# Kernel optimization log

Hardware: AMD Instinct MI355X
Metric: run time of the kernel (lower is better)

The kernel has to match this reference:

```python
import jax, jax.numpy as jnp
import numpy as np

NUM_GRAPHS = 64


def setup_inputs() -> dict:
    key = jax.random.key(0)
    ks = jax.random.split(key, 8)
    N, E, H, D_IN, NEXP = 100000, 1600000, 128, 4, 8
    atomic_numbers = jax.random.uniform(ks[0], (N,), dtype=jnp.float32) * 80.0
    pos = jax.random.normal(ks[1], (N, 3), dtype=jnp.float32)
    W0 = jax.random.normal(ks[2], (D_IN, H), dtype=jnp.float32) / np.sqrt(D_IN)
    b0 = jnp.zeros((H,), dtype=jnp.float32)
    W1 = jax.random.normal(ks[3], (H, H), dtype=jnp.float32) / np.sqrt(H)
    b1 = jnp.zeros((H,), dtype=jnp.float32)
    W2 = jax.random.normal(ks[4], (H, H), dtype=jnp.float32) / np.sqrt(H)
    b2 = jnp.zeros((H,), dtype=jnp.float32)
    lin_W = jax.random.normal(ks[5], (H, NEXP), dtype=jnp.float32) / np.sqrt(H)
    lin_b = jnp.zeros((NEXP,), dtype=jnp.float32)
    edge_index = jax.random.randint(ks[6], (2, E), 0, N, dtype=jnp.int64)
    batch = jnp.sort(jax.random.randint(ks[7], (N,), 0, NUM_GRAPHS, dtype=jnp.int64))
    return {
        "atomic_numbers": atomic_numbers, "pos": pos,
        "W0": W0, "b0": b0, "W1": W1, "b1": b1, "W2": W2, "b2": b2,
        "lin_W": lin_W, "lin_b": lin_b,
        "edge_index": edge_index, "batch": batch,
    }


def _gcn_layer(x, W, b, src, dst, norm, num_nodes):
    # GCNConv: transform, then symmetric-normalized scatter-aggregate (self-loops included in src/dst)
    h = x @ W                                   # [N, H]
    msg = h[src] * norm[:, None]                # [E+N, H] edge-gather
    out = jax.ops.segment_sum(msg, dst, num_segments=num_nodes)  # scatter-add at targets
    return out + b


def reference(atomic_numbers, pos, W0, b0, W1, b1, W2, b2, lin_W, lin_b, edge_index, batch):
    N = atomic_numbers.shape[0]
    x = jnp.concatenate([atomic_numbers[:, None], pos], axis=-1)  # [N, 4]

    # add self-loops (PyG GCNConv default)
    loop = jnp.arange(N, dtype=edge_index.dtype)
    src = jnp.concatenate([edge_index[0], loop])
    dst = jnp.concatenate([edge_index[1], loop])
    deg = jax.ops.segment_sum(jnp.ones_like(dst, dtype=jnp.float32), dst, num_segments=N)
    deg_inv_sqrt = jnp.where(deg > 0, deg ** -0.5, 0.0)
    norm = deg_inv_sqrt[src] * deg_inv_sqrt[dst]  # [E+N]

    for (W, b) in ((W0, b0), (W1, b1), (W2, b2)):
        x = _gcn_layer(x, W, b, src, dst, norm, N)
        x = jax.nn.relu(x)
        # dropout is identity at inference

    # global mean pool over graphs
    sums = jax.ops.segment_sum(x, batch, num_segments=NUM_GRAPHS)        # [G, H]
    counts = jax.ops.segment_sum(jnp.ones((N,), jnp.float32), batch, num_segments=NUM_GRAPHS)
    pooled = sums / jnp.maximum(counts, 1.0)[:, None]

    logits = pooled @ lin_W + lin_b             # [G, num_experts]
    return jax.nn.softmax(logits, axis=1)[:, :, None]  # [G, num_experts, 1]
```

## Files before the change

### kernel.cpp

```cpp
#include <hip/hip_runtime.h>
#include <math.h>

#define WG 256
#define NB 256
#define BSHIFT 9
#define NBLK 512

typedef float vf2 __attribute__((ext_vector_type(2)));
typedef short bf16x8 __attribute__((ext_vector_type(8)));
typedef float f32x4 __attribute__((ext_vector_type(4)));

#define XS_STRIDE 136
#define WT_STRIDE 136
#define C_STRIDE 132

__device__ __forceinline__ int lower_bound_i(const int* __restrict__ a, int n, int key) {
    int lo = 0, hi = n;
    while (lo < hi) { int mid = (lo + hi) >> 1; if (a[mid] < key) lo = mid + 1; else hi = mid; }
    return lo;
}

__device__ __forceinline__ void fp8x8_to_f8(uint2 raw, float* f) {
    vf2 a = __builtin_amdgcn_cvt_pk_f32_fp8((int)raw.x, false);
    vf2 b = __builtin_amdgcn_cvt_pk_f32_fp8((int)raw.x, true);
    vf2 c = __builtin_amdgcn_cvt_pk_f32_fp8((int)raw.y, false);
    vf2 d = __builtin_amdgcn_cvt_pk_f32_fp8((int)raw.y, true);
    f[0]=a.x; f[1]=a.y; f[2]=b.x; f[3]=b.y; f[4]=c.x; f[5]=c.y; f[6]=d.x; f[7]=d.y;
}
__device__ __forceinline__ unsigned int f4_to_fp8x4(float x, float y, float z, float w) {
    int v = __builtin_amdgcn_cvt_pk_fp8_f32(x, y, 0, false);
    v = __builtin_amdgcn_cvt_pk_fp8_f32(z, w, v, true);
    return (unsigned int)v;
}
__device__ __forceinline__ unsigned short f_to_bf_trunc(float f) {
    return (unsigned short)(__float_as_uint(f) >> 16);
}
__device__ __forceinline__ unsigned short f_to_bf_rne(float f) {
    unsigned int u = __float_as_uint(f);
    u += 0x7FFFu + ((u >> 16) & 1u);
    return (unsigned short)(u >> 16);
}


__global__ __launch_bounds__(256) void k_cnt(const int* __restrict__ edst, int E,
                                             int* __restrict__ gcounts) {
    __shared__ int hist[NB];
    int t = threadIdx.x, blk = blockIdx.x;
    if (t < NB) hist[t] = 0;
    __syncthreads();
    int chunk = (E + NBLK - 1) / NBLK;
    int e0 = blk * chunk, e1 = min(E, e0 + chunk);
    for (int e = e0 + t; e < e1; e += 256) atomicAdd(&hist[edst[e] >> BSHIFT], 1);
    __syncthreads();
    if (t < NB) gcounts[t * NBLK + blk] = hist[t];
}

__global__ __launch_bounds__(256) void k_scanA(int* __restrict__ gcounts,
                                               int* __restrict__ bsum) {
    __shared__ int wtot[4];
    int t = threadIdx.x;
    int base = blockIdx.x * 1024 + t * 4;
    int4 v = *(const int4*)&gcounts[base];
    int s = v.x + v.y + v.z + v.w;
    int lane = t & 63, wid = t >> 6;
    int x = s;
#pragma unroll
    for (int d = 1; d < 64; d <<= 1) { int y = __shfl_up(x, d); if (lane >= d) x += y; }
    if (lane == 63) wtot[wid] = x;
    __syncthreads();
    int woff = 0;
    for (int w = 0; w < wid; w++) woff += wtot[w];
    int excl = woff + x - s;
    int4 o;
    o.x = excl; o.y = excl + v.x; o.z = o.y + v.y; o.w = o.z + v.z;
    *(int4*)&gcounts[base] = o;
    if (t == 255) bsum[blockIdx.x] = woff + x;
}

__global__ void k_scanB(int* __restrict__ bsum) {
    __shared__ int sh[128];
    int t = threadIdx.x;
    int v = bsum[t];
    sh[t] = v;
    __syncthreads();
    for (int d = 1; d < 128; d <<= 1) {
        int a = (t >= d) ? sh[t - d] : 0;
        __syncthreads();
        sh[t] += a;
        __syncthreads();
    }
    bsum[t] = sh[t] - v;
}

__global__ __launch_bounds__(256) void k_scat(const int* __restrict__ esrc,
        const int* __restrict__ edst, int E,
        const int* __restrict__ gcounts, const int* __restrict__ bsum,
        int* __restrict__ pairs) {
    __shared__ int cur[NB];
    int t = threadIdx.x, blk = blockIdx.x;
    if (t < NB) {
        int idx = t * NBLK + blk;
        cur[t] = gcounts[idx] + bsum[idx >> 10];
    }
    __syncthreads();
    int chunk = (E + NBLK - 1) / NBLK;
    int e0 = blk * chunk, e1 = min(E, e0 + chunk);
    for (int e = e0 + t; e < e1; e += 256) {
        int d = edst[e], s = esrc[e];
        int pos = atomicAdd(&cur[d >> BSHIFT], 1);
        pairs[pos] = (s << BSHIFT) | (d & ((1 << BSHIFT) - 1));
    }
}

__global__ __launch_bounds__(256) void k_build(const int* __restrict__ pairs,
        const int* __restrict__ gcounts, const int* __restrict__ bsum, int N, int E,
        int* __restrict__ offs, int* __restrict__ srcs, float* __restrict__ dis) {
    __shared__ int cnt[512];
    __shared__ int wtot[4];
    int b = blockIdx.x, t = threadIdx.x;
    int n0 = b << BSHIFT;
    cnt[2 * t] = 0; cnt[2 * t + 1] = 0;
    __syncthreads();
    int i0 = b * NBLK, i1 = (b + 1) * NBLK;
    int bs = gcounts[i0] + bsum[i0 >> 10];
    int be = gcounts[i1] + bsum[i1 >> 10];
    int m = be - bs;
    const int* pb = &pairs[bs];
    for (int i = t; i < m; i += 256) {
        int p = pb[i];
        atomicAdd(&cnt[p & 511], 1);
    }
    __syncthreads();
    int v0 = cnt[2 * t], v1 = cnt[2 * t + 1];
    int ts = v0 + v1;
    int lane = t & 63, wid = t >> 6;
    int x = ts;
    #pragma unroll
    for (int d = 1; d < 64; d <<= 1) { int y = __shfl_up(x, d); if (lane >= d) x += y; }
    if (lane == 63) wtot[wid] = x;
    __syncthreads();
    int woff = 0;
    for (int w = 0; w < wid; w++) woff += wtot[w];
    int excl = woff + x - ts;
    int o0 = excl, o1 = excl + v0;
    cnt[2 * t] = o0; cnt[2 * t + 1] = o1;
    int n = n0 + 2 * t;
    if (n + 0 < N) { offs[n + 0] = bs + o0; dis[n + 0] = rsqrtf((float)(v0 + 1)); }
    if (n + 1 < N) { offs[n + 1] = bs + o1; dis[n + 1] = rsqrtf((float)(v1 + 1)); }
    if (b == gridDim.x - 1 && t == 255) offs[N] = E;
    __syncthreads();
    for (int i = t; i < m; i += 256) {
        int p = pb[i];
        int pos = atomicAdd(&cnt[p & 511], 1);
        srcs[bs + pos] = p >> BSHIFT;
    }
}

__global__ __launch_bounds__(256) void k_wt(const float* __restrict__ W,
                                            unsigned short* __restrict__ wt) {
    int idx = blockIdx.x * 256 + threadIdx.x;
    int k = idx >> 7, j = idx & 127;
    float v = W[k * 128 + j];
    wt[j * 128 + k] = f_to_bf_rne(v);
}


__global__ void k_l0(const float* __restrict__ an, const float* __restrict__ pos,
                     const float* __restrict__ W0, const float* __restrict__ dis,
                     unsigned int* __restrict__ h, int N) {
    int idx = blockIdx.x * blockDim.x + threadIdx.x;
    int n = idx >> 5, fq = idx & 31;
    if (n >= N) return;
    float a = an[n];
    float px = pos[n * 3 + 0], py = pos[n * 3 + 1], pz = pos[n * 3 + 2];
    float dn = dis[n];
    const float4 w0 = *(const float4*)&W0[0 * 128 + 4 * fq];
    const float4 w1 = *(const float4*)&W0[1 * 128 + 4 * fq];
    const float4 w2 = *(const float4*)&W0[2 * 128 + 4 * fq];
    const float4 w3 = *(const float4*)&W0[3 * 128 + 4 * fq];
    float4 r;
    r.x = (a * w0.x + px * w1.x + py * w2.x + pz * w3.x) * dn;
    r.y = (a * w0.y + px * w1.y + py * w2.y + pz * w3.y) * dn;
    r.z = (a * w0.z + px * w1.z + py * w2.z + pz * w3.z) * dn;
    r.w = (a * w0.w + px * w1.w + py * w2.w + pz * w3.w) * dn;
    h[(size_t)n * 32 + fq] = f4_to_fp8x4(r.x, r.y, r.z, r.w);
}

__global__ __launch_bounds__(256) void k_gemm(const unsigned int* __restrict__ x,
                                              const unsigned short* __restrict__ wt,
                                              const float* __restrict__ dis,
                                              unsigned int* __restrict__ h, int N) {
    __shared__ __align__(16) char ldsb[(64 * XS_STRIDE + 128 * WT_STRIDE) * 2];
    unsigned short* xs  = (unsigned short*)ldsb;
    unsigned short* wtl = xs + 64 * XS_STRIDE;
    float* Cs = (float*)ldsb;

    int t = threadIdx.x;
    int n0 = blockIdx.x * 64;

    {
        const uint2* xg = (const uint2*)(x + (size_t)n0 * 32);
        int validq = min(64, N - n0) * 16;
#pragma unroll
        for (int i = 0; i < 4; i++) {
            int idx = t + i * 256;
            int row = idx >> 4, part = idx & 15;
            float f[8];
            if (idx < validq) {
                fp8x8_to_f8(xg[idx], f);
#pragma unroll
                for (int k = 0; k < 8; k++) f[k] = fmaxf(f[k], 0.f);
            } else {
#pragma unroll
                for (int k = 0; k < 8; k++) f[k] = 0.f;
            }
            bf16x8 v;
#pragma unroll
            for (int k = 0; k < 8; k++) v[k] = (short)f_to_bf_trunc(f[k]);
            *(bf16x8*)&xs[row * XS_STRIDE + part * 8] = v;
        }
    }
    {
        const uint4* wg = (const uint4*)wt;
#pragma unroll
        for (int i = 0; i < 8; i++) {
            int idx = t + i * 256;
            int j = idx >> 4, part = idx & 15;
            uint4 v = wg[idx];
            *(uint4*)&wtl[j * WT_STRIDE + part * 8] = v;
        }
    }
    __syncthreads();

    int lane = t & 63, wv = t >> 6;
    int m = lane & 15, quad = lane >> 4;
    int rowbase = wv * 16;

    f32x4 acc[8];
#pragma unroll
    for (int c = 0; c < 8; c++) acc[c] = (f32x4){0.f, 0.f, 0.f, 0.f};

#pragma unroll
    for (int kt = 0; kt < 4; kt++) {
        bf16x8 a = *(bf16x8*)&xs[(rowbase + m) * XS_STRIDE + kt * 32 + quad * 8];
#pragma unroll
        for (int c = 0; c < 8; c++) {
            bf16x8 b = *(bf16x8*)&wtl[(c * 16 + m) * WT_STRIDE + kt * 32 + quad * 8];
            acc[c] = __builtin_amdgcn_mfma_f32_16x16x32_bf16(a, b, acc[c], 0, 0, 0);
        }
    }
    __syncthreads();

#pragma unroll
    for (int c = 0; c < 8; c++) {
#pragma unroll
        for (int r = 0; r < 4; r++) {
            Cs[(rowbase + quad * 4 + r) * C_STRIDE + c * 16 + m] = acc[c][r];
        }
    }
    __syncthreads();

    int fq = t & 31, ng = t >> 5;
#pragma unroll
    for (int i = 0; i < 8; i++) {
        int lrow = ng * 8 + i;
        int n = n0 + lrow;
        if (n < N) {
            float4 v = *(const float4*)&Cs[lrow * C_STRIDE + 4 * fq];
            float dn = dis[n];
            h[(size_t)n * 32 + fq] = f4_to_fp8x4(v.x * dn, v.y * dn, v.z * dn, v.w * dn);
        }
    }
}

__global__ __launch_bounds__(256) void k_agg(const unsigned int* __restrict__ h,
                      const float* __restrict__ bias,
                      const float* __restrict__ dis, const int* __restrict__ offs,
                      const int* __restrict__ srcs, unsigned int* __restrict__ agg, int N) {
    int fq = threadIdx.x & 15, ng = threadIdx.x >> 4;
    int n = blockIdx.x * 16 + ng;
    if (n >= N) return;
    const uint2* hp = (const uint2*)h;
    float acc[8], tmp[8];
    fp8x8_to_f8(hp[(size_t)n * 16 + fq], acc);
    int e0 = offs[n], e1 = offs[n + 1];
    int e = e0;
    for (; e + 8 <= e1; e += 8) {
        int s0 = srcs[e + 0], s1 = srcs[e + 1], s2 = srcs[e + 2], s3 = srcs[e + 3];
        int s4 = srcs[e + 4], s5 = srcs[e + 5], s6 = srcs[e + 6], s7 = srcs[e + 7];
        uint2 r0 = hp[(size_t)s0 * 16 + fq];
        uint2 r1 = hp[(size_t)s1 * 16 + fq];
        uint2 r2 = hp[(size_t)s2 * 16 + fq];
        uint2 r3 = hp[(size_t)s3 * 16 + fq];
        uint2 r4 = hp[(size_t)s4 * 16 + fq];
        uint2 r5 = hp[(size_t)s5 * 16 + fq];
        uint2 r6 = hp[(size_t)s6 * 16 + fq];
        uint2 r7 = hp[(size_t)s7 * 16 + fq];
        fp8x8_to_f8(r0, tmp);
#pragma unroll
        for (int k = 0; k < 8; k++) acc[k] += tmp[k];
        fp8x8_to_f8(r1, tmp);
#pragma unroll
        for (int k = 0; k < 8; k++) acc[k] += tmp[k];
        fp8x8_to_f8(r2, tmp);
#pragma unroll
        for (int k = 0; k < 8; k++) acc[k] += tmp[k];
        fp8x8_to_f8(r3, tmp);
#pragma unroll
        for (int k = 0; k < 8; k++) acc[k] += tmp[k];
        fp8x8_to_f8(r4, tmp);
#pragma unroll
        for (int k = 0; k < 8; k++) acc[k] += tmp[k];
        fp8x8_to_f8(r5, tmp);
#pragma unroll
        for (int k = 0; k < 8; k++) acc[k] += tmp[k];
        fp8x8_to_f8(r6, tmp);
#pragma unroll
        for (int k = 0; k < 8; k++) acc[k] += tmp[k];
        fp8x8_to_f8(r7, tmp);
#pragma unroll
        for (int k = 0; k < 8; k++) acc[k] += tmp[k];
    }
    for (; e < e1; ++e) {
        int s = srcs[e];
        fp8x8_to_f8(hp[(size_t)s * 16 + fq], tmp);
#pragma unroll
        for (int k = 0; k < 8; k++) acc[k] += tmp[k];
    }
    float dn = dis[n];
    const float4 bv0 = *(const float4*)&bias[8 * fq];
    const float4 bv1 = *(const float4*)&bias[8 * fq + 4];
    unsigned int lo = f4_to_fp8x4(bv0.x + dn * acc[0], bv0.y + dn * acc[1],
                                  bv0.z + dn * acc[2], bv0.w + dn * acc[3]);
    unsigned int hi = f4_to_fp8x4(bv1.x + dn * acc[4], bv1.y + dn * acc[5],
                                  bv1.z + dn * acc[6], bv1.w + dn * acc[7]);
    uint2 outv = make_uint2(lo, hi);
    *(uint2*)&agg[(size_t)n * 32 + 2 * fq] = outv;
}


__global__ void k_pool(const unsigned char* __restrict__ x, const int* __restrict__ batch,
                       float* __restrict__ pooled, int N) {
    int g = blockIdx.x >> 3, c = blockIdx.x & 7;
    int start = lower_bound_i(batch, N, g);
    int end   = lower_bound_i(batch, N, g + 1);
    int len = end - start;
    int cb = start + (int)((long)len * c / 8);
    int ce = start + (int)((long)len * (c + 1) / 8);
    int f = threadIdx.x & 127, half = threadIdx.x >> 7;
    float acc = 0.f;
    for (int n = cb + half; n < ce; n += 2) {
        int b = x[(size_t)n * 128 + f];
        vf2 v = __builtin_amdgcn_cvt_pk_f32_fp8(b, false);
        acc += fmaxf(v.x, 0.f);
    }
    __shared__ float sh[128];
    if (half == 1) sh[f] = acc;
    __syncthreads();
    if (half == 0) atomicAdd(&pooled[g * 128 + f], acc + sh[f]);
}

__global__ void k_head(const float* __restrict__ pooled, const int* __restrict__ batch,
                       const float* __restrict__ linW, const float* __restrict__ linb,
                       float* __restrict__ out, int N) {
    int g = threadIdx.x;
    if (g >= 64) return;
    int start = lower_bound_i(batch, N, g);
    int end   = lower_bound_i(batch, N, g + 1);
    float cnt = fmaxf((float)(end - start), 1.0f);
    float logits[8];
#pragma unroll
    for (int j = 0; j < 8; j++) logits[j] = linb[j];
    for (int f = 0; f < 128; f++) {
        float p = pooled[g * 128 + f] / cnt;
#pragma unroll
        for (int j = 0; j < 8; j++) logits[j] += p * linW[f * 8 + j];
    }
    float m = logits[0];
#pragma unroll
    for (int j = 1; j < 8; j++) m = fmaxf(m, logits[j]);
    float s = 0.f;
    float e[8];
#pragma unroll
    for (int j = 0; j < 8; j++) { e[j] = expf(logits[j] - m); s += e[j]; }
#pragma unroll
    for (int j = 0; j < 8; j++) out[g * 8 + j] = e[j] / s;
}


extern "C" void kernel_launch(void* const* d_in, const int* in_sizes, int n_in,
                              void* d_out, int out_size, void* d_ws, size_t ws_size,
                              hipStream_t stream) {
    const float* an   = (const float*)d_in[0];
    const float* pos  = (const float*)d_in[1];
    const float* W0   = (const float*)d_in[2];
    const float* b0   = (const float*)d_in[3];
    const float* W1   = (const float*)d_in[4];
    const float* b1   = (const float*)d_in[5];
    const float* W2   = (const float*)d_in[6];
    const float* b2   = (const float*)d_in[7];
    const float* linW = (const float*)d_in[8];
    const float* linb = (const float*)d_in[9];
    const int*   ei   = (const int*)d_in[10];
    const int*   batch= (const int*)d_in[11];

    int N = in_sizes[0];
    int E = in_sizes[10] / 2;
    const int* esrc = ei;
    const int* edst = ei + E;
    int nb = (N + (1 << BSHIFT) - 1) >> BSHIFT;

    char* p = (char*)d_ws;
    auto carve = [&](size_t bytes) -> void* {
        void* r = (void*)p;
        p += (bytes + 255) & ~(size_t)255;
        return r;
    };
    unsigned int* bufA = (unsigned int*)carve((size_t)N * 128);
    unsigned int* bufB = (unsigned int*)carve((size_t)N * 128);
    float* dis    = (float*)carve((size_t)N * 4);
    int*   offs   = (int*)  carve((size_t)(N + 1) * 4);
    int*   srcs   = (int*)  carve((size_t)E * 4);
    int*   pairs  = (int*)  carve((size_t)E * 4);
    int*   gcounts= (int*)  carve((size_t)NB * NBLK * 4);
    int*   bsum   = (int*)  carve(128 * 4);
    unsigned short* wt1 = (unsigned short*)carve(128 * 128 * 2);
    unsigned short* wt2 = (unsigned short*)carve(128 * 128 * 2);
    float* pooled = (float*)carve(64 * 128 * 4);

    hipMemsetAsync(pooled, 0, 64 * 128 * 4, stream);

    k_cnt  <<<NBLK, WG, 0, stream>>>(edst, E, gcounts);
    k_scanA<<<128, WG, 0, stream>>>(gcounts, bsum);
    k_scanB<<<1, 128, 0, stream>>>(bsum);
    k_scat <<<NBLK, WG, 0, stream>>>(esrc, edst, E, gcounts, bsum, pairs);
    k_build<<<nb, WG, 0, stream>>>(pairs, gcounts, bsum, N, E, offs, srcs, dis);

    k_wt<<<64, WG, 0, stream>>>(W1, wt1);
    k_wt<<<64, WG, 0, stream>>>(W2, wt2);

    k_l0  <<<((size_t)N * 32 + WG - 1) / WG, WG, 0, stream>>>(an, pos, W0, dis, bufA, N);
    k_agg <<<(N + 15) / 16, WG, 0, stream>>>(bufA, b0, dis, offs, srcs, bufB, N);
    k_gemm<<<(N + 63) / 64, WG, 0, stream>>>(bufB, wt1, dis, bufA, N);
    k_agg <<<(N + 15) / 16, WG, 0, stream>>>(bufA, b1, dis, offs, srcs, bufB, N);
    k_gemm<<<(N + 63) / 64, WG, 0, stream>>>(bufB, wt2, dis, bufA, N);
    k_agg <<<(N + 15) / 16, WG, 0, stream>>>(bufA, b2, dis, offs, srcs, bufB, N);

    k_pool<<<64 * 8, WG, 0, stream>>>((const unsigned char*)bufB, batch, pooled, N);
    k_head<<<1, 64, 0, stream>>>(pooled, batch, linW, linb, (float*)d_out, N);
}
```

Measured before the change: 346.8 us.

## Fuse neighbor aggregation into GEMM prologue and widen aggregation loads to 16 bytes

Aggregation for layers 0 and 1 now happens inside the GEMM kernel. Each workgroup gathers its 64 rows' neighbor sums, applies bias and ReLU, and writes bf16 rows straight into LDS, so the fp8 aggregated intermediate is no longer written to and reread from global memory. Aggregation loads widen from 8 to 16 bytes per lane, with 8 lanes per node and an unroll of 4. The scan stage is also shrunk to 256 partition blocks, with a single-wave shuffle scan replacing the LDS scan. A risk is that the GEMM blocks now carry irregular gather latency while holding a large LDS footprint, which may lower occupancy during the gather phase.

```diff
diff --git a/kernel.cpp b/kernel.cpp
--- a/kernel.cpp
+++ b/kernel.cpp
@@ -4,7 +4,7 @@
 #define WG 256
 #define NB 256
 #define BSHIFT 9
-#define NBLK 512
+#define NBLK 256
 
 typedef float vf2 __attribute__((ext_vector_type(2)));
 typedef short bf16x8 __attribute__((ext_vector_type(8)));
@@ -26,6 +26,12 @@
     vf2 c = __builtin_amdgcn_cvt_pk_f32_fp8((int)raw.y, false);
     vf2 d = __builtin_amdgcn_cvt_pk_f32_fp8((int)raw.y, true);
     f[0]=a.x; f[1]=a.y; f[2]=b.x; f[3]=b.y; f[4]=c.x; f[5]=c.y; f[6]=d.x; f[7]=d.y;
+}
+__device__ __forceinline__ void fp8x16_to_f(uint4 raw, float* f) {
+    uint2 lo, hi;
+    lo.x = raw.x; lo.y = raw.y; hi.x = raw.z; hi.y = raw.w;
+    fp8x8_to_f8(lo, f);
+    fp8x8_to_f8(hi, f + 8);
 }
 __device__ __forceinline__ unsigned int f4_to_fp8x4(float x, float y, float z, float w) {
     int v = __builtin_amdgcn_cvt_pk_fp8_f32(x, y, 0, false);
@@ -78,18 +84,12 @@
 }
 
 __global__ void k_scanB(int* __restrict__ bsum) {
-    __shared__ int sh[128];
     int t = threadIdx.x;
     int v = bsum[t];
-    sh[t] = v;
-    __syncthreads();
-    for (int d = 1; d < 128; d <<= 1) {
-        int a = (t >= d) ? sh[t - d] : 0;
-        __syncthreads();
-        sh[t] += a;
-        __syncthreads();
-    }
-    bsum[t] = sh[t] - v;
+    int x = v;
+#pragma unroll
+    for (int d = 1; d < 64; d <<= 1) { int y = __shfl_up(x, d); if (t >= d) x += y; }
+    bsum[t] = x - v;
 }
 
 __global__ __launch_bounds__(256) void k_scat(const int* __restrict__ esrc,
@@ -186,10 +186,10 @@
     h[(size_t)n * 32 + fq] = f4_to_fp8x4(r.x, r.y, r.z, r.w);
 }
 
-__global__ __launch_bounds__(256) void k_gemm(const unsigned int* __restrict__ x,
-                                              const unsigned short* __restrict__ wt,
-                                              const float* __restrict__ dis,
-                                              unsigned int* __restrict__ h, int N) {
+__global__ __launch_bounds__(256) void k_fused(const unsigned int* __restrict__ x,
+        const float* __restrict__ bias, const unsigned short* __restrict__ wt,
+        const float* __restrict__ dis, const int* __restrict__ offs,
+        const int* __restrict__ srcs, unsigned int* __restrict__ h, int N) {
     __shared__ __align__(16) char ldsb[(64 * XS_STRIDE + 128 * WT_STRIDE) * 2];
     unsigned short* xs  = (unsigned short*)ldsb;
     unsigned short* wtl = xs + 64 * XS_STRIDE;
@@ -198,28 +198,6 @@
     int t = threadIdx.x;
     int n0 = blockIdx.x * 64;
 
-    {
-        const uint2* xg = (const uint2*)(x + (size_t)n0 * 32);
-        int validq = min(64, N - n0) * 16;
-#pragma unroll
-        for (int i = 0; i < 4; i++) {
-            int idx = t + i * 256;
-            int row = idx >> 4, part = idx & 15;
-            float f[8];
-            if (idx < validq) {
-                fp8x8_to_f8(xg[idx], f);
-#pragma unroll
-                for (int k = 0; k < 8; k++) f[k] = fmaxf(f[k], 0.f);
-            } else {
-#pragma unroll
-                for (int k = 0; k < 8; k++) f[k] = 0.f;
-            }
-            bf16x8 v;
-#pragma unroll
-            for (int k = 0; k < 8; k++) v[k] = (short)f_to_bf_trunc(f[k]);
-            *(bf16x8*)&xs[row * XS_STRIDE + part * 8] = v;
-        }
-    }
     {
         const uint4* wg = (const uint4*)wt;
 #pragma unroll
@@ -228,6 +206,68 @@
             int j = idx >> 4, part = idx & 15;
             uint4 v = wg[idx];
             *(uint4*)&wtl[j * WT_STRIDE + part * 8] = v;
+        }
+    }
+
+    {
+        const uint4* hp4 = (const uint4*)x;
+        int fq = t & 7, ng = t >> 3;
+        float bv[16];
+        *(float4*)&bv[0]  = *(const float4*)&bias[fq * 16 + 0];
+        *(float4*)&bv[4]  = *(const float4*)&bias[fq * 16 + 4];
+        *(float4*)&bv[8]  = *(const float4*)&bias[fq * 16 + 8];
+        *(float4*)&bv[12] = *(const float4*)&bias[fq * 16 + 12];
+#pragma unroll
+        for (int half = 0; half < 2; half++) {
+            int lrow = half * 32 + ng;
+            int n = n0 + lrow;
+            float out[16];
+            if (n < N) {
+                float acc[16], tmp[16];
+                fp8x16_to_f(hp4[(size_t)n * 8 + fq], acc);
+                int e0 = offs[n], e1 = offs[n + 1];
+                int e = e0;
+                for (; e + 4 <= e1; e += 4) {
+                    int s0 = srcs[e + 0], s1 = srcs[e + 1];
+                    int s2 = srcs[e + 2], s3 = srcs[e + 3];
+                    uint4 r0 = hp4[(size_t)s0 * 8 + fq];
+                    uint4 r1 = hp4[(size_t)s1 * 8 + fq];
+                    uint4 r2 = hp4[(size_t)s2 * 8 + fq];
+                    uint4 r3 = hp4[(size_t)s3 * 8 + fq];
+                    fp8x16_to_f(r0, tmp);
+#pragma unroll
+                    for (int k = 0; k < 16; k++) acc[k] += tmp[k];
+                    fp8x16_to_f(r1, tmp);
+#pragma unroll
+                    for (int k = 0; k < 16; k++) acc[k] += tmp[k];
+                    fp8x16_to_f(r2, tmp);
+#pragma unroll
+                    for (int k = 0; k < 16; k++) acc[k] += tmp[k];
+                    fp8x16_to_f(r3, tmp);
+#pragma unroll
+                    for (int k = 0; k < 16; k++) acc[k] += tmp[k];
+                }
+                for (; e < e1; ++e) {
+                    int s = srcs[e];
+                    fp8x16_to_f(hp4[(size_t)s * 8 + fq], tmp);
+#pragma unroll
+                    for (int k = 0; k < 16; k++) acc[k] += tmp[k];
+                }
+                float dn = dis[n];
+#pragma unroll
+                for (int k = 0; k < 16; k++) out[k] = fmaxf(bv[k] + dn * acc[k], 0.f);
+            } else {
+#pragma unroll
+                for (int k = 0; k < 16; k++) out[k] = 0.f;
+            }
+            bf16x8 v0, v1;
+#pragma unroll
+            for (int k = 0; k < 8; k++) {
+                v0[k] = (short)f_to_bf_rne(out[k]);
+                v1[k] = (short)f_to_bf_rne(out[k + 8]);
+            }
+            *(bf16x8*)&xs[lrow * XS_STRIDE + fq * 16] = v0;
+            *(bf16x8*)&xs[lrow * XS_STRIDE + fq * 16 + 8] = v1;
         }
     }
     __syncthreads();
@@ -277,65 +317,54 @@
                       const float* __restrict__ bias,
                       const float* __restrict__ dis, const int* __restrict__ offs,
                       const int* __restrict__ srcs, unsigned int* __restrict__ agg, int N) {
-    int fq = threadIdx.x & 15, ng = threadIdx.x >> 4;
-    int n = blockIdx.x * 16 + ng;
+    int fq = threadIdx.x & 7, ng = threadIdx.x >> 3;
+    int n = blockIdx.x * 32 + ng;
     if (n >= N) return;
-    const uint2* hp = (const uint2*)h;
-    float acc[8], tmp[8];
-    fp8x8_to_f8(hp[(size_t)n * 16 + fq], acc);
+    const uint4* hp4 = (const uint4*)h;
+    float acc[16], tmp[16];
+    fp8x16_to_f(hp4[(size_t)n * 8 + fq], acc);
     int e0 = offs[n], e1 = offs[n + 1];
     int e = e0;
-    for (; e + 8 <= e1; e += 8) {
+    for (; e + 4 <= e1; e += 4) {
         int s0 = srcs[e + 0], s1 = srcs[e + 1], s2 = srcs[e + 2], s3 = srcs[e + 3];
-        int s4 = srcs[e + 4], s5 = srcs[e + 5], s6 = srcs[e + 6], s7 = srcs[e + 7];
-        uint2 r0 = hp[(size_t)s0 * 16 + fq];
-        uint2 r1 = hp[(size_t)s1 * 16 + fq];
-        uint2 r2 = hp[(size_t)s2 * 16 + fq];
-        uint2 r3 = hp[(size_t)s3 * 16 + fq];
-        uint2 r4 = hp[(size_t)s4 * 16 + fq];
-        uint2 r5 = hp[(size_t)s5 * 16 + fq];
-        uint2 r6 = hp[(size_t)s6 * 16 + fq];
-        uint2 r7 = hp[(size_t)s7 * 16 + fq];
-        fp8x8_to_f8(r0, tmp);
-#pragma unroll
-        for (int k = 0; k < 8; k++) acc[k] += tmp[k];
-        fp8x8_to_f8(r1, tmp);
-#pragma unroll
-        for (int k = 0; k < 8; k++) acc[k] += tmp[k];
-        fp8x8_to_f8(r2, tmp);
-#pragma unroll
-        for (int k = 0; k < 8; k++) acc[k] += tmp[k];
-        fp8x8_to_f8(r3, tmp);
-#pragma unroll
-        for (int k = 0; k < 8; k++) acc[k] += tmp[k];
-        fp8x8_to_f8(r4, tmp);
-#pragma unroll
-        for (int k = 0; k < 8; k++) acc[k] += tmp[k];
-        fp8x8_to_f8(r5, tmp);
-#pragma unroll
-        for (int k = 0; k < 8; k++) acc[k] += tmp[k];
-        fp8x8_to_f8(r6, tmp);
-#pragma unroll
-        for (int k = 0; k < 8; k++) acc[k] += tmp[k];
-        fp8x8_to_f8(r7, tmp);
-#pragma unroll
-        for (int k = 0; k < 8; k++) acc[k] += tmp[k];
+        uint4 r0 = hp4[(size_t)s0 * 8 + fq];
+        uint4 r1 = hp4[(size_t)s1 * 8 + fq];
+        uint4 r2 = hp4[(size_t)s2 * 8 + fq];
+        uint4 r3 = hp4[(size_t)s3 * 8 + fq];
+        fp8x16_to_f(r0, tmp);
+#pragma unroll
+        for (int k = 0; k < 16; k++) acc[k] += tmp[k];
+        fp8x16_to_f(r1, tmp);
+#pragma unroll
+        for (int k = 0; k < 16; k++) acc[k] += tmp[k];
+        fp8x16_to_f(r2, tmp);
+#pragma unroll
+        for (int k = 0; k < 16; k++) acc[k] += tmp[k];
+        fp8x16_to_f(r3, tmp);
+#pragma unroll
+        for (int k = 0; k < 16; k++) acc[k] += tmp[k];
     }
     for (; e < e1; ++e) {
         int s = srcs[e];
-        fp8x8_to_f8(hp[(size_t)s * 16 + fq], tmp);
-#pragma unroll
-        for (int k = 0; k < 8; k++) acc[k] += tmp[k];
+        fp8x16_to_f(hp4[(size_t)s * 8 + fq], tmp);
+#pragma unroll
+        for (int k = 0; k < 16; k++) acc[k] += tmp[k];
     }
     float dn = dis[n];
-    const float4 bv0 = *(const float4*)&bias[8 * fq];
-    const float4 bv1 = *(const float4*)&bias[8 * fq + 4];
-    unsigned int lo = f4_to_fp8x4(bv0.x + dn * acc[0], bv0.y + dn * acc[1],
-                                  bv0.z + dn * acc[2], bv0.w + dn * acc[3]);
-    unsigned int hi = f4_to_fp8x4(bv1.x + dn * acc[4], bv1.y + dn * acc[5],
-                                  bv1.z + dn * acc[6], bv1.w + dn * acc[7]);
-    uint2 outv = make_uint2(lo, hi);
-    *(uint2*)&agg[(size_t)n * 32 + 2 * fq] = outv;
+    float bv[16];
+    *(float4*)&bv[0]  = *(const float4*)&bias[fq * 16 + 0];
+    *(float4*)&bv[4]  = *(const float4*)&bias[fq * 16 + 4];
+    *(float4*)&bv[8]  = *(const float4*)&bias[fq * 16 + 8];
+    *(float4*)&bv[12] = *(const float4*)&bias[fq * 16 + 12];
+    float o[16];
+#pragma unroll
+    for (int k = 0; k < 16; k++) o[k] = bv[k] + dn * acc[k];
+    uint4 outv;
+    outv.x = f4_to_fp8x4(o[0], o[1], o[2], o[3]);
+    outv.y = f4_to_fp8x4(o[4], o[5], o[6], o[7]);
+    outv.z = f4_to_fp8x4(o[8], o[9], o[10], o[11]);
+    outv.w = f4_to_fp8x4(o[12], o[13], o[14], o[15]);
+    *(uint4*)&agg[(size_t)n * 32 + fq * 4] = outv;
 }
 
 
@@ -423,7 +452,7 @@
     int*   srcs   = (int*)  carve((size_t)E * 4);
     int*   pairs  = (int*)  carve((size_t)E * 4);
     int*   gcounts= (int*)  carve((size_t)NB * NBLK * 4);
-    int*   bsum   = (int*)  carve(128 * 4);
+    int*   bsum   = (int*)  carve(64 * 4);
     unsigned short* wt1 = (unsigned short*)carve(128 * 128 * 2);
     unsigned short* wt2 = (unsigned short*)carve(128 * 128 * 2);
     float* pooled = (float*)carve(64 * 128 * 4);
@@ -431,20 +460,18 @@
     hipMemsetAsync(pooled, 0, 64 * 128 * 4, stream);
 
     k_cnt  <<<NBLK, WG, 0, stream>>>(edst, E, gcounts);
-    k_scanA<<<128, WG, 0, stream>>>(gcounts, bsum);
-    k_scanB<<<1, 128, 0, stream>>>(bsum);
+    k_scanA<<<(NB * NBLK) / 1024, WG, 0, stream>>>(gcounts, bsum);
+    k_scanB<<<1, 64, 0, stream>>>(bsum);
     k_scat <<<NBLK, WG, 0, stream>>>(esrc, edst, E, gcounts, bsum, pairs);
     k_build<<<nb, WG, 0, stream>>>(pairs, gcounts, bsum, N, E, offs, srcs, dis);
 
     k_wt<<<64, WG, 0, stream>>>(W1, wt1);
     k_wt<<<64, WG, 0, stream>>>(W2, wt2);
 
-    k_l0  <<<((size_t)N * 32 + WG - 1) / WG, WG, 0, stream>>>(an, pos, W0, dis, bufA, N);
-    k_agg <<<(N + 15) / 16, WG, 0, stream>>>(bufA, b0, dis, offs, srcs, bufB, N);
-    k_gemm<<<(N + 63) / 64, WG, 0, stream>>>(bufB, wt1, dis, bufA, N);
-    k_agg <<<(N + 15) / 16, WG, 0, stream>>>(bufA, b1, dis, offs, srcs, bufB, N);
-    k_gemm<<<(N + 63) / 64, WG, 0, stream>>>(bufB, wt2, dis, bufA, N);
-    k_agg <<<(N + 15) / 16, WG, 0, stream>>>(bufA, b2, dis, offs, srcs, bufB, N);
+    k_l0   <<<((size_t)N * 32 + WG - 1) / WG, WG, 0, stream>>>(an, pos, W0, dis, bufA, N);
+    k_fused<<<(N + 63) / 64, WG, 0, stream>>>(bufA, b0, wt1, dis, offs, srcs, bufB, N);
+    k_fused<<<(N + 63) / 64, WG, 0, stream>>>(bufB, b1, wt2, dis, offs, srcs, bufA, N);
+    k_agg  <<<(N + 31) / 32, WG, 0, stream>>>(bufA, b2, dis, offs, srcs, bufB, N);
 
     k_pool<<<64 * 8, WG, 0, stream>>>((const unsigned char*)bufB, batch, pooled, N);
     k_head<<<1, 64, 0, stream>>>(pooled, batch, linW, linb, (float*)d_out, N);
```

Result: no change. 342.6 us (-1.2%).
